# Optimization experiments

Measured on AMD Instinct MI355X. Metric: run time of the kernel, lower is better.

The kernel has to match this reference:

```python
import jax, jax.numpy as jnp
import numpy as np

OUT = 2048          # rows of sparse weight (out_features)
IN = 2048           # cols of sparse weight (in_features)
NNZ_PER_ROW = 128   # uniform nnz per row -> simple valid CSR indptr
NNZ = OUT * NNZ_PER_ROW
N = 512             # number of input rows (tokens)


def setup_inputs() -> dict:
    key = jax.random.key(0)
    k1, k2, k3 = jax.random.split(key, 3)
    x = jax.random.normal(k1, (N, IN), dtype=jnp.float32)
    data = jax.random.normal(k2, (NNZ,), dtype=jnp.float32)
    # sorted column indices per row (canonical-ish CSR; duplicates are harmless, they sum)
    indices = jnp.sort(
        jax.random.randint(k3, (OUT, NNZ_PER_ROW), 0, IN), axis=1
    ).reshape(NNZ).astype(jnp.int32)
    indptr = (jnp.arange(OUT + 1) * NNZ_PER_ROW).astype(jnp.int32)
    return {"x": x, "data": data, "indices": indices, "indptr": indptr}


def reference(x, data, indices, indptr):
    # CuPyLinear.forward: result = (W_csr @ x.T).T, i.e. y = x @ W.T with W sparse CSR.
    nnz = data.shape[0]
    n_rows = indptr.shape[0] - 1  # static
    # expand CSR indptr to per-nnz row ids
    rows = jnp.searchsorted(indptr, jnp.arange(nnz, dtype=indptr.dtype), side="right") - 1
    # contrib[k, n] = data[k] * x[n, col[k]]
    contrib = data[:, None] * x.T[indices]                 # [nnz, N]
    y_t = jax.ops.segment_sum(contrib, rows, num_segments=n_rows)  # [out, N]
    return y_t.T                                           # [N, out]
```

## Files before the change

### kernel.cpp

```cpp
#include <hip/hip_runtime.h>

#define N_TOK 512
#define IN_F  2048
#define OUT_F 2048
#define NNZ_ROW 128

#define ROW_G 4
#define TOK_G 256

__device__ ushort g_xT16[IN_F * N_TOK];

static __device__ __forceinline__ ushort f2bf(float f) {
    unsigned u = __float_as_uint(f);
    unsigned r = (u + 0x7fffu + ((u >> 16) & 1u)) >> 16;
    return (ushort)r;
}

__global__ __launch_bounds__(256) void transpose_x(const float* __restrict__ x) {
    __shared__ float tile[32][33];
    const int bx = blockIdx.x;
    const int by = blockIdx.y;
    const int tx = threadIdx.x;
    const int ty = threadIdx.y;

    const int col  = bx * 32 + tx;
    const int row0 = by * 32 + ty;
#pragma unroll
    for (int j = 0; j < 32; j += 8)
        tile[ty + j][tx] = x[(row0 + j) * IN_F + col];
    __syncthreads();

    const int n  = by * 32 + tx;
    const int c0 = bx * 32 + ty;
#pragma unroll
    for (int j = 0; j < 32; j += 8)
        g_xT16[(c0 + j) * N_TOK + n] = f2bf(tile[tx][ty + j]);
}

__global__ __launch_bounds__(256) void spmm_csr(const float* __restrict__ data,
                                                const int*   __restrict__ indices,
                                                const int*   __restrict__ indptr,
                                                float*       __restrict__ y) {
    const int rg = blockIdx.x;
    const int tg = blockIdx.y;
    const int r0 = rg * ROW_G;
    const int t  = threadIdx.x;

    __shared__ int2  s_wi[ROW_G * NNZ_ROW];
    __shared__ float ytile[ROW_G][TOK_G + 4];

#pragma unroll
    for (int i = 0; i < 2; ++i) {
        const int g    = t + i * 256;
        const int rl   = g >> 7;
        const int off  = g & (NNZ_ROW - 1);
        const int base = indptr[r0 + rl] + off;
        s_wi[g] = make_int2(indices[base] * (N_TOK / 4), __float_as_int(data[base]));
    }
    __syncthreads();

    const uint2* __restrict__ xT2 = (const uint2*)g_xT16;
    const int w = t >> 6;
    const int l = t & 63;
    const int tokoff = tg * (TOK_G / 4) + l;

    const int2* __restrict__ p = &s_wi[w * NNZ_ROW];
    float4 acc = make_float4(0.f, 0.f, 0.f, 0.f);
#pragma unroll 16
    for (int k = 0; k < NNZ_ROW; ++k) {
        const int2 wi  = p[k];
        const int  off = __builtin_amdgcn_readfirstlane(wi.x);
        const float wt = __int_as_float(__builtin_amdgcn_readfirstlane(wi.y));
        const uint2 u  = xT2[off + tokoff];
        acc.x += wt * __uint_as_float(u.x << 16);
        acc.y += wt * __uint_as_float(u.x);
        acc.z += wt * __uint_as_float(u.y << 16);
        acc.w += wt * __uint_as_float(u.y);
    }
    *(float4*)&ytile[w][4 * l] = acc;
    __syncthreads();

    const int n0 = tg * TOK_G;
#pragma unroll
    for (int i = 0; i < 4; ++i) {
        const int g = t + i * 256;
        const int n = g >> 2;
        const int f = g & (ROW_G - 1);
        y[(n0 + n) * OUT_F + r0 + f] = ytile[f][n];
    }
}

extern "C" void kernel_launch(void* const* d_in, const int* in_sizes, int n_in,
                              void* d_out, int out_size, void* d_ws, size_t ws_size,
                              hipStream_t stream) {
    const float* x       = (const float*)d_in[0];
    const float* data    = (const float*)d_in[1];
    const int*   indices = (const int*)  d_in[2];
    const int*   indptr  = (const int*)  d_in[3];
    float*       y       = (float*)d_out;

    dim3 tb(32, 8);
    dim3 tg(IN_F / 32, N_TOK / 32);
    transpose_x<<<tg, tb, 0, stream>>>(x);

    dim3 sg(OUT_F / ROW_G, N_TOK / TOK_G);
    spmm_csr<<<sg, 256, 0, stream>>>(data, indices, indptr, y);
}
```

Before: 81.50 us.

## Pipeline x gathers into LDS with global_load_lds and cover all tokens per block

```diff
diff --git a/kernel.cpp b/kernel.cpp
--- a/kernel.cpp
+++ b/kernel.cpp
@@ -6,7 +6,7 @@
 #define NNZ_ROW 128
 
 #define ROW_G 4
-#define TOK_G 256
+#define DEPTH 8
 
 __device__ ushort g_xT16[IN_F * N_TOK];
 
@@ -42,12 +42,12 @@
                                                 const int*   __restrict__ indptr,
                                                 float*       __restrict__ y) {
     const int rg = blockIdx.x;
-    const int tg = blockIdx.y;
     const int r0 = rg * ROW_G;
     const int t  = threadIdx.x;
 
     __shared__ int2  s_wi[ROW_G * NNZ_ROW];
-    __shared__ float ytile[ROW_G][TOK_G + 4];
+    __shared__ float ytile[ROW_G][N_TOK + 4];
+    __shared__ uint4 slots[ROW_G][DEPTH][64];
 
 #pragma unroll
     for (int i = 0; i < 2; ++i) {
@@ -55,38 +55,74 @@
         const int rl   = g >> 7;
         const int off  = g & (NNZ_ROW - 1);
         const int base = indptr[r0 + rl] + off;
-        s_wi[g] = make_int2(indices[base] * (N_TOK / 4), __float_as_int(data[base]));
+        s_wi[g] = make_int2(indices[base], __float_as_int(data[base]));
     }
     __syncthreads();
 
-    const uint2* __restrict__ xT2 = (const uint2*)g_xT16;
     const int w = t >> 6;
     const int l = t & 63;
-    const int tokoff = tg * (TOK_G / 4) + l;
+    const int2* __restrict__ p = &s_wi[w * NNZ_ROW];
+    const char* __restrict__ xl = (const char*)g_xT16 + (l << 4);
+    uint4* const myslots = &slots[w][0][0];
 
-    const int2* __restrict__ p = &s_wi[w * NNZ_ROW];
-    float4 acc = make_float4(0.f, 0.f, 0.f, 0.f);
-#pragma unroll 16
-    for (int k = 0; k < NNZ_ROW; ++k) {
-        const int2 wi  = p[k];
-        const int  off = __builtin_amdgcn_readfirstlane(wi.x);
-        const float wt = __int_as_float(__builtin_amdgcn_readfirstlane(wi.y));
-        const uint2 u  = xT2[off + tokoff];
-        acc.x += wt * __uint_as_float(u.x << 16);
-        acc.y += wt * __uint_as_float(u.x);
-        acc.z += wt * __uint_as_float(u.y << 16);
-        acc.w += wt * __uint_as_float(u.y);
+#pragma unroll
+    for (int k = 0; k < DEPTH; ++k) {
+        const int col = __builtin_amdgcn_readfirstlane(p[k].x);
+        __builtin_amdgcn_global_load_lds(
+            (const unsigned*)(xl + (col << 10)),
+            (unsigned*)(myslots + k * 64), 16, 0, 0);
     }
-    *(float4*)&ytile[w][4 * l] = acc;
+
+    float acc[8];
+#pragma unroll
+    for (int j = 0; j < 8; ++j) acc[j] = 0.f;
+
+#pragma unroll 8
+    for (int k = 0; k < NNZ_ROW - DEPTH; ++k) {
+        asm volatile("s_waitcnt vmcnt(7)" ::: "memory");
+        __builtin_amdgcn_sched_barrier(0);
+        const uint4 u  = myslots[(k & 7) * 64 + l];
+        const float wt = __int_as_float(__builtin_amdgcn_readfirstlane(p[k].y));
+        acc[0] += wt * __uint_as_float(u.x << 16);
+        acc[1] += wt * __uint_as_float(u.x);
+        acc[2] += wt * __uint_as_float(u.y << 16);
+        acc[3] += wt * __uint_as_float(u.y);
+        acc[4] += wt * __uint_as_float(u.z << 16);
+        acc[5] += wt * __uint_as_float(u.z);
+        acc[6] += wt * __uint_as_float(u.w << 16);
+        acc[7] += wt * __uint_as_float(u.w);
+        const int col = __builtin_amdgcn_readfirstlane(p[k + DEPTH].x);
+        __builtin_amdgcn_global_load_lds(
+            (const unsigned*)(xl + (col << 10)),
+            (unsigned*)(myslots + (k & 7) * 64), 16, 0, 0);
+    }
+
+    asm volatile("s_waitcnt vmcnt(0)" ::: "memory");
+    __builtin_amdgcn_sched_barrier(0);
+#pragma unroll
+    for (int k = NNZ_ROW - DEPTH; k < NNZ_ROW; ++k) {
+        const uint4 u  = myslots[(k & 7) * 64 + l];
+        const float wt = __int_as_float(__builtin_amdgcn_readfirstlane(p[k].y));
+        acc[0] += wt * __uint_as_float(u.x << 16);
+        acc[1] += wt * __uint_as_float(u.x);
+        acc[2] += wt * __uint_as_float(u.y << 16);
+        acc[3] += wt * __uint_as_float(u.y);
+        acc[4] += wt * __uint_as_float(u.z << 16);
+        acc[5] += wt * __uint_as_float(u.z);
+        acc[6] += wt * __uint_as_float(u.w << 16);
+        acc[7] += wt * __uint_as_float(u.w);
+    }
+
+    *(float4*)&ytile[w][8 * l]     = make_float4(acc[0], acc[1], acc[2], acc[3]);
+    *(float4*)&ytile[w][8 * l + 4] = make_float4(acc[4], acc[5], acc[6], acc[7]);
     __syncthreads();
 
-    const int n0 = tg * TOK_G;
 #pragma unroll
-    for (int i = 0; i < 4; ++i) {
+    for (int i = 0; i < 8; ++i) {
         const int g = t + i * 256;
         const int n = g >> 2;
         const int f = g & (ROW_G - 1);
-        y[(n0 + n) * OUT_F + r0 + f] = ytile[f][n];
+        y[n * OUT_F + r0 + f] = ytile[f][n];
     }
 }
 
@@ -103,6 +139,5 @@
     dim3 tg(IN_F / 32, N_TOK / 32);
     transpose_x<<<tg, tb, 0, stream>>>(x);
 
-    dim3 sg(OUT_F / ROW_G, N_TOK / TOK_G);
-    spmm_csr<<<sg, 256, 0, stream>>>(data, indices, indptr, y);
+    spmm_csr<<<dim3(OUT_F / ROW_G), 256, 0, stream>>>(data, indices, indptr, y);
 }
```

Result: no change. 81.86 us (+0.4%).

## Stage token slabs of bf16 x in LDS and gather from shared memory

Applied to the files above, without the earlier changes.

```diff
diff --git a/kernel.cpp b/kernel.cpp
--- a/kernel.cpp
+++ b/kernel.cpp
@@ -5,88 +5,110 @@
 #define OUT_F 2048
 #define NNZ_ROW 128
 
-#define ROW_G 4
-#define TOK_G 256
+#define SLAB_TOK 16
+#define NSLAB (N_TOK / SLAB_TOK)
 
-__device__ ushort g_xT16[IN_F * N_TOK];
+#define ROWS_B 128
+#define YP 18
+
+__device__ ushort g_xs[NSLAB * IN_F * SLAB_TOK];
 
 static __device__ __forceinline__ ushort f2bf(float f) {
     unsigned u = __float_as_uint(f);
-    unsigned r = (u + 0x7fffu + ((u >> 16) & 1u)) >> 16;
-    return (ushort)r;
+    return (ushort)((u + 0x7fffu + ((u >> 16) & 1u)) >> 16);
 }
 
-__global__ __launch_bounds__(256) void transpose_x(const float* __restrict__ x) {
-    __shared__ float tile[32][33];
-    const int bx = blockIdx.x;
-    const int by = blockIdx.y;
-    const int tx = threadIdx.x;
-    const int ty = threadIdx.y;
+__global__ __launch_bounds__(256) void tile_x(const float* __restrict__ x) {
+    __shared__ float tile[16][130];
+    const int s  = blockIdx.y;
+    const int c0 = blockIdx.x * 128;
+    const int t  = threadIdx.x;
 
-    const int col  = bx * 32 + tx;
-    const int row0 = by * 32 + ty;
+    {
+        const int col = t & 127;
+        const int rh  = t >> 7;
 #pragma unroll
-    for (int j = 0; j < 32; j += 8)
-        tile[ty + j][tx] = x[(row0 + j) * IN_F + col];
+        for (int i = 0; i < 8; ++i) {
+            const int row = i * 2 + rh;
+            tile[row][col] = x[(size_t)(s * SLAB_TOK + row) * IN_F + c0 + col];
+        }
+    }
+    __syncthreads();
+    {
+        const int lc   = t >> 1;
+        const int half = t & 1;
+        unsigned o[4];
+#pragma unroll
+        for (int j = 0; j < 4; ++j) {
+            const ushort a = f2bf(tile[half * 8 + 2 * j][lc]);
+            const ushort b = f2bf(tile[half * 8 + 2 * j + 1][lc]);
+            o[j] = (unsigned)a | ((unsigned)b << 16);
+        }
+        ushort* dst = g_xs + ((size_t)s * IN_F + c0 + lc) * SLAB_TOK + half * 8;
+        *(uint4*)dst = make_uint4(o[0], o[1], o[2], o[3]);
+    }
+}
+
+__global__ __launch_bounds__(512, 4) void spmm(const float* __restrict__ data,
+                                               const int*   __restrict__ indices,
+                                               const int*   __restrict__ indptr,
+                                               float*       __restrict__ y) {
+    __shared__ ushort s_x[IN_F * SLAB_TOK];
+    __shared__ float  s_y[ROWS_B * YP];
+
+    const int rg   = blockIdx.x;
+    const int slab = blockIdx.y;
+    const int r0   = rg * ROWS_B;
+    const int t    = threadIdx.x;
+
+    const char* src = (const char*)g_xs + (size_t)slab * (IN_F * SLAB_TOK * 2);
+#pragma unroll
+    for (int i = 0; i < (IN_F * SLAB_TOK * 2 / 16) / 512; ++i) {
+        const int off = (t + i * 512) * 16;
+        __builtin_amdgcn_global_load_lds((const unsigned*)(src + off),
+                                         (unsigned*)((char*)s_x + off), 16, 0, 0);
+    }
+
+    const int w  = t >> 6;
+    const int l  = t & 63;
+    const int g  = l >> 3;
+    const int tl = l & 7;
+    const int lr = (w * 8 + g) * 2;
+    const int base = indptr[r0];
+    const unsigned* sxw = (const unsigned*)s_x;
+
     __syncthreads();
 
-    const int n  = by * 32 + tx;
-    const int c0 = bx * 32 + ty;
 #pragma unroll
-    for (int j = 0; j < 32; j += 8)
-        g_xT16[(c0 + j) * N_TOK + n] = f2bf(tile[tx][ty + j]);
-}
-
-__global__ __launch_bounds__(256) void spmm_csr(const float* __restrict__ data,
-                                                const int*   __restrict__ indices,
-                                                const int*   __restrict__ indptr,
-                                                float*       __restrict__ y) {
-    const int rg = blockIdx.x;
-    const int tg = blockIdx.y;
-    const int r0 = rg * ROW_G;
-    const int t  = threadIdx.x;
-
-    __shared__ int2  s_wi[ROW_G * NNZ_ROW];
-    __shared__ float ytile[ROW_G][TOK_G + 4];
-
-#pragma unroll
-    for (int i = 0; i < 2; ++i) {
-        const int g    = t + i * 256;
-        const int rl   = g >> 7;
-        const int off  = g & (NNZ_ROW - 1);
-        const int base = indptr[r0 + rl] + off;
-        s_wi[g] = make_int2(indices[base] * (N_TOK / 4), __float_as_int(data[base]));
+    for (int rr = 0; rr < 2; ++rr) {
+        const int r = lr + rr;
+        const int4*   ip = (const int4*)(indices + base + r * NNZ_ROW);
+        const float4* dp = (const float4*)(data    + base + r * NNZ_ROW);
+        float a0 = 0.f, a1 = 0.f;
+#pragma unroll 2
+        for (int c = 0; c < NNZ_ROW / 8; ++c) {
+            const int4   i0 = ip[2 * c], i1 = ip[2 * c + 1];
+            const float4 d0 = dp[2 * c], d1 = dp[2 * c + 1];
+            unsigned v;
+            v = sxw[i0.x * 8 + tl]; a0 += d0.x * __uint_as_float(v << 16); a1 += d0.x * __uint_as_float(v);
+            v = sxw[i0.y * 8 + tl]; a0 += d0.y * __uint_as_float(v << 16); a1 += d0.y * __uint_as_float(v);
+            v = sxw[i0.z * 8 + tl]; a0 += d0.z * __uint_as_float(v << 16); a1 += d0.z * __uint_as_float(v);
+            v = sxw[i0.w * 8 + tl]; a0 += d0.w * __uint_as_float(v << 16); a1 += d0.w * __uint_as_float(v);
+            v = sxw[i1.x * 8 + tl]; a0 += d1.x * __uint_as_float(v << 16); a1 += d1.x * __uint_as_float(v);
+            v = sxw[i1.y * 8 + tl]; a0 += d1.y * __uint_as_float(v << 16); a1 += d1.y * __uint_as_float(v);
+            v = sxw[i1.z * 8 + tl]; a0 += d1.z * __uint_as_float(v << 16); a1 += d1.z * __uint_as_float(v);
+            v = sxw[i1.w * 8 + tl]; a0 += d1.w * __uint_as_float(v << 16); a1 += d1.w * __uint_as_float(v);
+        }
+        *(float2*)&s_y[r * YP + tl * 2] = make_float2(a0, a1);
     }
     __syncthreads();
 
-    const uint2* __restrict__ xT2 = (const uint2*)g_xT16;
-    const int w = t >> 6;
-    const int l = t & 63;
-    const int tokoff = tg * (TOK_G / 4) + l;
-
-    const int2* __restrict__ p = &s_wi[w * NNZ_ROW];
-    float4 acc = make_float4(0.f, 0.f, 0.f, 0.f);
-#pragma unroll 16
-    for (int k = 0; k < NNZ_ROW; ++k) {
-        const int2 wi  = p[k];
-        const int  off = __builtin_amdgcn_readfirstlane(wi.x);
-        const float wt = __int_as_float(__builtin_amdgcn_readfirstlane(wi.y));
-        const uint2 u  = xT2[off + tokoff];
-        acc.x += wt * __uint_as_float(u.x << 16);
-        acc.y += wt * __uint_as_float(u.x);
-        acc.z += wt * __uint_as_float(u.y << 16);
-        acc.w += wt * __uint_as_float(u.y);
-    }
-    *(float4*)&ytile[w][4 * l] = acc;
-    __syncthreads();
-
-    const int n0 = tg * TOK_G;
 #pragma unroll
     for (int i = 0; i < 4; ++i) {
-        const int g = t + i * 256;
-        const int n = g >> 2;
-        const int f = g & (ROW_G - 1);
-        y[(n0 + n) * OUT_F + r0 + f] = ytile[f][n];
+        const int idx = t + i * 512;
+        const int nn  = idx >> 7;
+        const int r   = idx & 127;
+        y[(size_t)(slab * SLAB_TOK + nn) * OUT_F + r0 + r] = s_y[r * YP + nn];
     }
 }
 
@@ -99,10 +121,7 @@
     const int*   indptr  = (const int*)  d_in[3];
     float*       y       = (float*)d_out;
 
-    dim3 tb(32, 8);
-    dim3 tg(IN_F / 32, N_TOK / 32);
-    transpose_x<<<tg, tb, 0, stream>>>(x);
-
-    dim3 sg(OUT_F / ROW_G, N_TOK / TOK_G);
-    spmm_csr<<<sg, 256, 0, stream>>>(data, indices, indptr, y);
+    tile_x<<<dim3(IN_F / 128, NSLAB), 256, 0, stream>>>(x);
+    spmm<<<dim3(OUT_F / ROWS_B, NSLAB), 512, 0, stream>>>(
+        data, indices, indptr, y);
 }
```

After: 83.78 us. 2.8% more time.
